# Kernel optimization log

Hardware: AMD Instinct MI355X
Metric: run time of the kernel (lower is better)

Reference implementation:

```python
import jax, jax.numpy as jnp
import numpy as np

N, E, D, K = 50000, 600000, 128, 8
EPS = 1e-09


def setup_inputs() -> dict:
    key = jax.random.key(0)
    ks = jax.random.split(key, 10)
    feature = jax.random.normal(ks[0], (N, D), dtype=jnp.float32)
    snorm_n = jax.random.uniform(ks[1], (N, 1), dtype=jnp.float32)
    src = jax.random.randint(ks[2], (E,), 0, N, dtype=jnp.int32)
    dst = jax.random.randint(ks[3], (E,), 0, N, dtype=jnp.int32)
    W_low = jax.random.normal(ks[4], (D, D), dtype=jnp.float32) / np.sqrt(D)
    W_high = jax.random.normal(ks[5], (D, D), dtype=jnp.float32) / np.sqrt(D)
    W_mid = jax.random.normal(ks[6], (D, D), dtype=jnp.float32) / np.sqrt(D)
    gamma_low = jax.random.uniform(ks[7], (K,), dtype=jnp.float32)
    gamma_high = jax.random.uniform(ks[8], (K,), dtype=jnp.float32)
    gamma_mid = jax.random.uniform(ks[9], (K,), dtype=jnp.float32)
    bias = jnp.zeros((D,), dtype=jnp.float32)
    return {"feature": feature, "snorm_n": snorm_n, "src": src, "dst": dst,
            "W_low": W_low, "W_high": W_high, "W_mid": W_mid,
            "gamma_low": gamma_low, "gamma_high": gamma_high,
            "gamma_mid": gamma_mid, "bias": bias}


def _mp(feat, src, dst, norm):
    # symmetric-normalized SpMM: h[v] = norm[v] * sum_{u->v} norm[u]*feat[u]
    msg = (feat * norm[:, None])[src]                        # [E, D] gather
    agg = jax.ops.segment_sum(msg, dst, num_segments=N)       # [N, D] scatter-add
    return agg * norm[:, None]


def reference(feature, snorm_n, src, dst, W_low, W_high, W_mid,
              gamma_low, gamma_high, gamma_mid, bias):
    deg = jax.ops.segment_sum(jnp.ones((E,), feature.dtype), dst, num_segments=N)
    norm = jnp.clip(deg, 1.0) ** -0.5                          # in-degree^-0.5
    alpha = jnp.linspace(EPS, 1.0 - EPS, K).astype(feature.dtype)
    midalpha = jnp.linspace(EPS, 1.0, K).astype(feature.dtype)

    h = _mp(feature, src, dst, norm)

    gl = jax.nn.relu(gamma_low)
    o0 = (jnp.dot(alpha, gl) * h + jnp.dot(1.0 - alpha, gl) * feature) @ W_low.T
    gh = jax.nn.relu(gamma_high)
    o1 = (jnp.dot(-alpha, gh) * h + jnp.dot(1.0 - alpha, gh) * feature) @ W_high.T
    gm = jax.nn.relu(gamma_mid)
    h1 = _mp(h, src, dst, norm)
    o2 = (jnp.sum(gm) * h1 - jnp.dot(midalpha, gm) * feature) @ W_mid.T

    # sequential mutual gating, exactly as the torch in-place updates
    o0 = o0 * jax.nn.sigmoid(o1 + o2)
    o1 = o1 * jax.nn.sigmoid(o0 + o2)
    o2 = o2 * jax.nn.sigmoid(o0 + o1)

    out = o0 + o1 + o2 + bias
    out = out * snorm_n          # graph_norm
    out = jax.nn.relu(out)       # activation
    return out
```

## Files before the change

### kernel.cpp

```cpp
#include <hip/hip_runtime.h>
#include <hip/hip_bf16.h>
#include <math.h>

#define N_NODES 50000
#define N_EDGES 600000
#define DIM 128
#define KGAM 8
#define EPSV 1e-9f
#define RBLK 3128
#define NTILES 1564
#define GGRID 512

typedef __attribute__((ext_vector_type(8))) short short8;
typedef __attribute__((ext_vector_type(4))) float float4v;

__device__ __forceinline__ short f2bf(float f) {
    return (short)__builtin_bit_cast(unsigned short, __float2bfloat16(f));
}
__device__ __forceinline__ unsigned int pack2(float a, float b) {
    return (unsigned int)(unsigned short)f2bf(a) | ((unsigned int)(unsigned short)f2bf(b) << 16);
}
__device__ __forceinline__ float sigm(float x) { return 1.f / (1.f + __expf(-x)); }

__global__ void k_deg(const int* __restrict__ dst, int* __restrict__ deg) {
    int e = blockIdx.x * blockDim.x + threadIdx.x;
    if (e < N_EDGES) atomicAdd(&deg[dst[e]], 1);
}

__global__ void k_scan1(const int* __restrict__ deg, int* __restrict__ rowstart,
                        int* __restrict__ bsums, float* __restrict__ norm) {
    __shared__ int s[256];
    int tid = threadIdx.x;
    int i0 = blockIdx.x * 1024 + tid * 4;
    int v[4]; int sum = 0;
#pragma unroll
    for (int c = 0; c < 4; ++c) {
        int i = i0 + c;
        int d = (i < N_NODES) ? deg[i] : 0;
        v[c] = d; sum += d;
    }
    s[tid] = sum; __syncthreads();
#pragma unroll
    for (int off = 1; off < 256; off <<= 1) {
        int t = (tid >= off) ? s[tid - off] : 0;
        __syncthreads();
        s[tid] += t;
        __syncthreads();
    }
    if (tid == 255) bsums[blockIdx.x] = s[255];
    int run = s[tid] - sum;
#pragma unroll
    for (int c = 0; c < 4; ++c) {
        int i = i0 + c;
        if (i < N_NODES) {
            rowstart[i] = run;
            norm[i] = rsqrtf((float)(v[c] < 1 ? 1 : v[c]));
        }
        run += v[c];
    }
}

__global__ void k_scan2(int* __restrict__ bsums, int nb) {
    __shared__ int s[64];
    int tid = threadIdx.x;
    int v = (tid < nb) ? bsums[tid] : 0;
    s[tid] = v; __syncthreads();
#pragma unroll
    for (int off = 1; off < 64; off <<= 1) {
        int t = (tid >= off) ? s[tid - off] : 0;
        __syncthreads();
        s[tid] += t;
        __syncthreads();
    }
    if (tid < nb) bsums[tid] = s[tid] - v;
}

__global__ void k_scan3(const int* __restrict__ bsums, int* __restrict__ rowstart) {
    int i = blockIdx.x * blockDim.x + threadIdx.x;
    if (i < N_NODES) rowstart[i] += bsums[i >> 10];
    if (i == 0) rowstart[N_NODES] = N_EDGES;
}

__global__ void k_fill(const int* __restrict__ src, const int* __restrict__ dst,
                       const int* __restrict__ rowstart, int* __restrict__ cnt,
                       int* __restrict__ esrc) {
    int e = blockIdx.x * blockDim.x + threadIdx.x;
    if (e < N_EDGES) {
        int d = dst[e];
        int slot = rowstart[d] + atomicAdd(&cnt[d], 1);
        esrc[slot] = src[e];
    }
}

__global__ void k_wconv(const float* __restrict__ W0, const float* __restrict__ W1,
                        const float* __restrict__ W2, const float* __restrict__ gl,
                        const float* __restrict__ gh, const float* __restrict__ gm,
                        unsigned int* __restrict__ Wb) {
    int g = blockIdx.y;
    float a0 = 0, b0 = 0, a1 = 0, b1 = 0, sg = 0, m2 = 0;
#pragma unroll
    for (int k = 0; k < KGAM; ++k) {
        float al = EPSV + (float)k * (1.f - 2.f * EPSV) / (KGAM - 1);
        float md = EPSV + (float)k * (1.f - EPSV) / (KGAM - 1);
        float l = fmaxf(gl[k], 0.f), h = fmaxf(gh[k], 0.f), m = fmaxf(gm[k], 0.f);
        a0 += al * l;  b0 += (1.f - al) * l;
        a1 += -al * h; b1 += (1.f - al) * h;
        sg += m;       m2 += md * m;
    }
    float cc[6] = {a0, b0, a1, b1, sg, -m2};
    float c = cc[g];
    const float* Ws = (g < 2) ? W0 : (g < 4) ? W1 : W2;
    int i = (blockIdx.x * 256 + threadIdx.x) * 4;
    if (i < DIM * DIM) {
        float4 v = *(const float4*)(Ws + i);
        uint2 o; o.x = pack2(c * v.x, c * v.y); o.y = pack2(c * v.z, c * v.w);
        *(uint2*)(Wb + (g * DIM * DIM + i) / 2) = o;
    }
}

__device__ __forceinline__ size_t tiled_off(int row, int k) {
    return (size_t)(row >> 4) * 2048 + ((k >> 5) << 9) + (((k >> 3) & 3) << 7)
         + ((row & 15) << 3) + (k & 7);
}

__global__ void k_prescale(const float4* __restrict__ f, const float* __restrict__ norm,
                           unsigned int* __restrict__ fb, uint2* __restrict__ fp) {
    int i = blockIdx.x * 256 + threadIdx.x;
    if (i >= N_NODES * DIM / 4) return;
    int row = i >> 5;
    int k0 = (i & 31) * 4;
    float nv = norm[row];
    float4 v = f[i];
    uint2 a; a.x = pack2(v.x, v.y); a.y = pack2(v.z, v.w);
    uint2 b; b.x = pack2(v.x * nv, v.y * nv); b.y = pack2(v.z * nv, v.w * nv);
    *(uint2*)(fb + tiled_off(row, k0) / 2) = a;
    fp[i] = b;
}

__device__ __forceinline__ void acc8(float* a, uint4 r) {
    a[0] += __builtin_bit_cast(float, r.x << 16);
    a[1] += __builtin_bit_cast(float, r.x & 0xffff0000u);
    a[2] += __builtin_bit_cast(float, r.y << 16);
    a[3] += __builtin_bit_cast(float, r.y & 0xffff0000u);
    a[4] += __builtin_bit_cast(float, r.z << 16);
    a[5] += __builtin_bit_cast(float, r.z & 0xffff0000u);
    a[6] += __builtin_bit_cast(float, r.w << 16);
    a[7] += __builtin_bit_cast(float, r.w & 0xffff0000u);
}

__global__ void k_spmm(const uint4* __restrict__ in, const float* __restrict__ norm,
                       const int* __restrict__ rowstart, const int* __restrict__ esrc,
                       uint4* __restrict__ hout, uint4* __restrict__ preout, int wpre) {
    int v = blockIdx.x * 16 + (threadIdx.x >> 4);
    int l = threadIdx.x & 15;
    if (v >= N_NODES) return;
    int beg = rowstart[v], end = rowstart[v + 1];
    float a[8] = {0.f, 0.f, 0.f, 0.f, 0.f, 0.f, 0.f, 0.f};
    int t = beg;
    for (; t + 7 < end; t += 8) {
        int u0 = esrc[t],     u1 = esrc[t + 1], u2 = esrc[t + 2], u3 = esrc[t + 3];
        int u4 = esrc[t + 4], u5 = esrc[t + 5], u6 = esrc[t + 6], u7 = esrc[t + 7];
        uint4 r0 = in[(size_t)u0 * 16 + l];
        uint4 r1 = in[(size_t)u1 * 16 + l];
        uint4 r2 = in[(size_t)u2 * 16 + l];
        uint4 r3 = in[(size_t)u3 * 16 + l];
        uint4 r4 = in[(size_t)u4 * 16 + l];
        uint4 r5 = in[(size_t)u5 * 16 + l];
        uint4 r6 = in[(size_t)u6 * 16 + l];
        uint4 r7 = in[(size_t)u7 * 16 + l];
        acc8(a, r0); acc8(a, r1); acc8(a, r2); acc8(a, r3);
        acc8(a, r4); acc8(a, r5); acc8(a, r6); acc8(a, r7);
    }
    if (t + 3 < end) {
        int u0 = esrc[t], u1 = esrc[t + 1], u2 = esrc[t + 2], u3 = esrc[t + 3];
        uint4 r0 = in[(size_t)u0 * 16 + l];
        uint4 r1 = in[(size_t)u1 * 16 + l];
        uint4 r2 = in[(size_t)u2 * 16 + l];
        uint4 r3 = in[(size_t)u3 * 16 + l];
        acc8(a, r0); acc8(a, r1); acc8(a, r2); acc8(a, r3);
        t += 4;
    }
    if (t + 1 < end) {
        int u0 = esrc[t], u1 = esrc[t + 1];
        uint4 r0 = in[(size_t)u0 * 16 + l];
        uint4 r1 = in[(size_t)u1 * 16 + l];
        acc8(a, r0); acc8(a, r1);
        t += 2;
    }
    if (t < end) {
        uint4 r = in[(size_t)esrc[t] * 16 + l];
        acc8(a, r);
    }
    float nv = norm[v];
    uint4 o;
    o.x = pack2(a[0] * nv, a[1] * nv); o.y = pack2(a[2] * nv, a[3] * nv);
    o.z = pack2(a[4] * nv, a[5] * nv); o.w = pack2(a[6] * nv, a[7] * nv);
    size_t tix = (size_t)(v >> 4) * 256 + (size_t)(l >> 2) * 64
               + (size_t)(l & 3) * 16 + (v & 15);
    hout[tix] = o;
    if (wpre) {
        float n2 = nv * nv;
        uint4 p;
        p.x = pack2(a[0] * n2, a[1] * n2); p.y = pack2(a[2] * n2, a[3] * n2);
        p.z = pack2(a[4] * n2, a[5] * n2); p.w = pack2(a[6] * n2, a[7] * n2);
        preout[(size_t)v * 16 + l] = p;
    }
}

typedef const __attribute__((address_space(1))) unsigned int* gp1_t;
typedef __attribute__((address_space(3))) unsigned int* lp3_t;

__global__ __launch_bounds__(512, 2) void k_gemm_fused(
    const short* __restrict__ hB, const short* __restrict__ fB,
    const short* __restrict__ h1B, const short* __restrict__ Wb,
    const float* __restrict__ bias, const float* __restrict__ snorm,
    float* __restrict__ out) {
    __shared__ short Ts[2][24 * 512];

    const int tid = threadIdx.x;
    const int lane = tid & 63;
    const int wv = tid >> 6;
    const int m = lane & 15;
    const int quad = lane >> 4;

    const int col = wv * 16 + m;
    const float bc = bias[col];
    const short* wp = Wb + (size_t)col * DIM + quad * 8;

    int t0 = blockIdx.x;
    {
#pragma unroll
        for (int i = 0; i < 3; ++i) {
            int s = wv * 3 + i;
            int g = s >> 3, rb = (s >> 2) & 1, ks = s & 3;
            const short* base = (g == 0) ? hB : (g == 1) ? fB : h1B;
            const short* gp = base + (size_t)(t0 * 2 + rb) * 2048 + ks * 512 + lane * 8;
            __builtin_amdgcn_global_load_lds((gp1_t)(const void*)gp,
                                             (lp3_t)(void*)&Ts[0][s * 512], 16, 0, 0);
        }
    }

    int buf = 0;
    for (int t = t0; t < NTILES; t += GGRID) {
        __syncthreads();

        int tn = t + GGRID;
        if (tn < NTILES) {
#pragma unroll
            for (int i = 0; i < 3; ++i) {
                int s = wv * 3 + i;
                int g = s >> 3, rb = (s >> 2) & 1, ks = s & 3;
                const short* base = (g == 0) ? hB : (g == 1) ? fB : h1B;
                const short* gp = base + (size_t)(tn * 2 + rb) * 2048 + ks * 512 + lane * 8;
                __builtin_amdgcn_global_load_lds((gp1_t)(const void*)gp,
                                                 (lp3_t)(void*)&Ts[buf ^ 1][s * 512], 16, 0, 0);
            }
        }

        float4v acc[3][2];
        const float4v zero = {0.f, 0.f, 0.f, 0.f};
#pragma unroll
        for (int g = 0; g < 3; ++g) {
            acc[g][0] = zero; acc[g][1] = zero;
        }

#pragma unroll
        for (int ks = 0; ks < 4; ++ks) {
            const short* wk = wp + ks * 32;
            short8 b0 = *(const short8*)(wk);
            short8 b1 = *(const short8*)(wk + DIM * DIM);
            short8 b2 = *(const short8*)(wk + 2 * DIM * DIM);
            short8 b3 = *(const short8*)(wk + 3 * DIM * DIM);
            short8 b4 = *(const short8*)(wk + 4 * DIM * DIM);
            short8 b5 = *(const short8*)(wk + 5 * DIM * DIM);
#pragma unroll
            for (int rb = 0; rb < 2; ++rb) {
                const short* ap = &Ts[buf][(rb * 4 + ks) * 512 + lane * 8];
                short8 x_h = *(const short8*)(ap);
                short8 x_f = *(const short8*)(ap + 8 * 512);
                short8 x_1 = *(const short8*)(ap + 16 * 512);
                acc[0][rb] = __builtin_amdgcn_mfma_f32_16x16x32_bf16(x_h, b0, acc[0][rb], 0, 0, 0);
                acc[0][rb] = __builtin_amdgcn_mfma_f32_16x16x32_bf16(x_f, b1, acc[0][rb], 0, 0, 0);
                acc[1][rb] = __builtin_amdgcn_mfma_f32_16x16x32_bf16(x_h, b2, acc[1][rb], 0, 0, 0);
                acc[1][rb] = __builtin_amdgcn_mfma_f32_16x16x32_bf16(x_f, b3, acc[1][rb], 0, 0, 0);
                acc[2][rb] = __builtin_amdgcn_mfma_f32_16x16x32_bf16(x_1, b4, acc[2][rb], 0, 0, 0);
                acc[2][rb] = __builtin_amdgcn_mfma_f32_16x16x32_bf16(x_f, b5, acc[2][rb], 0, 0, 0);
            }
        }

#pragma unroll
        for (int rb = 0; rb < 2; ++rb) {
#pragma unroll
            for (int r = 0; r < 4; ++r) {
                int row = t * 32 + rb * 16 + quad * 4 + r;
                if (row < N_NODES) {
                    float sn = snorm[row];
                    float o0 = acc[0][rb][r], o1 = acc[1][rb][r], o2 = acc[2][rb][r];
                    float g0 = o0 * sigm(o1 + o2);
                    float g1 = o1 * sigm(g0 + o2);
                    float g2 = o2 * sigm(g0 + g1);
                    float vv = (g0 + g1 + g2 + bc) * sn;
                    out[(size_t)row * DIM + col] = fmaxf(vv, 0.f);
                }
            }
        }
        buf ^= 1;
    }
}

extern "C" void kernel_launch(void* const* d_in, const int* in_sizes, int n_in,
                              void* d_out, int out_size, void* d_ws, size_t ws_size,
                              hipStream_t stream) {
    const float* feature = (const float*)d_in[0];
    const float* snorm   = (const float*)d_in[1];
    const int*   src     = (const int*)d_in[2];
    const int*   dst     = (const int*)d_in[3];
    const float* W_low   = (const float*)d_in[4];
    const float* W_high  = (const float*)d_in[5];
    const float* W_mid   = (const float*)d_in[6];
    const float* gl      = (const float*)d_in[7];
    const float* gh      = (const float*)d_in[8];
    const float* gm      = (const float*)d_in[9];
    const float* bias    = (const float*)d_in[10];
    float* out = (float*)d_out;

    char* w = (char*)d_ws;
    auto alloc = [&](size_t bytes) {
        char* p = w;
        w += (bytes + 255) & ~(size_t)255;
        return p;
    };
    const size_t tiledBytes = (size_t)RBLK * 2048 * 2;
    float* norm   = (float*)alloc((size_t)N_NODES * 4);
    int* deg      = (int*)alloc((size_t)2 * N_NODES * 4);
    int* cnt      = deg + N_NODES;
    int* rowstart = (int*)alloc((size_t)(N_NODES + 1) * 4);
    int* bsums    = (int*)alloc(64 * 4);
    int* esrc     = (int*)alloc((size_t)N_EDGES * 4);
    short* Wb     = (short*)alloc((size_t)6 * DIM * DIM * 2);
    short* fb     = (short*)alloc(tiledBytes);
    short* fp     = (short*)alloc((size_t)N_NODES * DIM * 2);
    short* h      = (short*)alloc(tiledBytes);
    short* hp     = (short*)alloc((size_t)N_NODES * DIM * 2);
    short* h1     = (short*)alloc(tiledBytes);

    hipMemsetAsync(deg, 0, (size_t)2 * N_NODES * 4, stream);
    k_deg<<<(N_EDGES + 255) / 256, 256, 0, stream>>>(dst, deg);
    int nchunks = (N_NODES + 1023) / 1024;
    k_scan1<<<nchunks, 256, 0, stream>>>(deg, rowstart, bsums, norm);
    k_scan2<<<1, 64, 0, stream>>>(bsums, nchunks);
    k_scan3<<<(N_NODES + 255) / 256, 256, 0, stream>>>(bsums, rowstart);
    k_fill<<<(N_EDGES + 255) / 256, 256, 0, stream>>>(src, dst, rowstart, cnt, esrc);
    k_wconv<<<dim3(16, 6), 256, 0, stream>>>(W_low, W_high, W_mid, gl, gh, gm,
                                             (unsigned int*)Wb);
    k_prescale<<<(N_NODES * DIM / 4 + 255) / 256, 256, 0, stream>>>(
        (const float4*)feature, norm, (unsigned int*)fb, (uint2*)fp);

    int spmm_blocks = (N_NODES + 15) / 16;
    k_spmm<<<spmm_blocks, 256, 0, stream>>>((const uint4*)fp, norm, rowstart, esrc,
                                            (uint4*)h, (uint4*)hp, 1);
    k_spmm<<<spmm_blocks, 256, 0, stream>>>((const uint4*)hp, norm, rowstart, esrc,
                                            (uint4*)h1, (uint4*)hp, 0);

    k_gemm_fused<<<GGRID, 512, 0, stream>>>(h, fb, h1, Wb, bias, snorm, out);
}
```

Before: 252.9 us.

## Split SpMM edges across wavefront subgroups and use one-tile-per-block GEMM

The SpMM now gives each node a full 64-lane wavefront. Four 16-lane groups each take an interleaved subset of the node's edges, and their partial sums are combined with cross-lane shuffles. This is meant to spread uneven in-degrees and expose more memory-level parallelism per node, at the cost of shuffle reductions and idle lanes on low-degree nodes. The fused GEMM drops the persistent double-buffered loop for a non-persistent grid of 256-thread blocks, one 32-row tile each, with each wave computing two column blocks. This trades prefetch overlap for higher occupancy and simpler scheduling.

```diff
diff --git a/kernel.cpp b/kernel.cpp
--- a/kernel.cpp
+++ b/kernel.cpp
@@ -9,7 +9,6 @@
 #define EPSV 1e-9f
 #define RBLK 3128
 #define NTILES 1564
-#define GGRID 512
 
 typedef __attribute__((ext_vector_type(8))) short short8;
 typedef __attribute__((ext_vector_type(4))) float float4v;
@@ -151,122 +150,97 @@
 __global__ void k_spmm(const uint4* __restrict__ in, const float* __restrict__ norm,
                        const int* __restrict__ rowstart, const int* __restrict__ esrc,
                        uint4* __restrict__ hout, uint4* __restrict__ preout, int wpre) {
-    int v = blockIdx.x * 16 + (threadIdx.x >> 4);
-    int l = threadIdx.x & 15;
+    int v = blockIdx.x * 4 + (threadIdx.x >> 6);
     if (v >= N_NODES) return;
+    int lane = threadIdx.x & 63;
+    int eg = lane >> 4;
+    int l = lane & 15;
     int beg = rowstart[v], end = rowstart[v + 1];
     float a[8] = {0.f, 0.f, 0.f, 0.f, 0.f, 0.f, 0.f, 0.f};
-    int t = beg;
-    for (; t + 7 < end; t += 8) {
-        int u0 = esrc[t],     u1 = esrc[t + 1], u2 = esrc[t + 2], u3 = esrc[t + 3];
-        int u4 = esrc[t + 4], u5 = esrc[t + 5], u6 = esrc[t + 6], u7 = esrc[t + 7];
-        uint4 r0 = in[(size_t)u0 * 16 + l];
-        uint4 r1 = in[(size_t)u1 * 16 + l];
-        uint4 r2 = in[(size_t)u2 * 16 + l];
-        uint4 r3 = in[(size_t)u3 * 16 + l];
-        uint4 r4 = in[(size_t)u4 * 16 + l];
-        uint4 r5 = in[(size_t)u5 * 16 + l];
-        uint4 r6 = in[(size_t)u6 * 16 + l];
-        uint4 r7 = in[(size_t)u7 * 16 + l];
-        acc8(a, r0); acc8(a, r1); acc8(a, r2); acc8(a, r3);
-        acc8(a, r4); acc8(a, r5); acc8(a, r6); acc8(a, r7);
-    }
-    if (t + 3 < end) {
-        int u0 = esrc[t], u1 = esrc[t + 1], u2 = esrc[t + 2], u3 = esrc[t + 3];
-        uint4 r0 = in[(size_t)u0 * 16 + l];
-        uint4 r1 = in[(size_t)u1 * 16 + l];
-        uint4 r2 = in[(size_t)u2 * 16 + l];
-        uint4 r3 = in[(size_t)u3 * 16 + l];
-        acc8(a, r0); acc8(a, r1); acc8(a, r2); acc8(a, r3);
-        t += 4;
-    }
-    if (t + 1 < end) {
-        int u0 = esrc[t], u1 = esrc[t + 1];
+    int e = beg + eg;
+    for (; e + 4 < end; e += 8) {
+        int u0 = esrc[e], u1 = esrc[e + 4];
         uint4 r0 = in[(size_t)u0 * 16 + l];
         uint4 r1 = in[(size_t)u1 * 16 + l];
         acc8(a, r0); acc8(a, r1);
-        t += 2;
-    }
-    if (t < end) {
-        uint4 r = in[(size_t)esrc[t] * 16 + l];
+    }
+    if (e < end) {
+        uint4 r = in[(size_t)esrc[e] * 16 + l];
         acc8(a, r);
     }
-    float nv = norm[v];
-    uint4 o;
-    o.x = pack2(a[0] * nv, a[1] * nv); o.y = pack2(a[2] * nv, a[3] * nv);
-    o.z = pack2(a[4] * nv, a[5] * nv); o.w = pack2(a[6] * nv, a[7] * nv);
-    size_t tix = (size_t)(v >> 4) * 256 + (size_t)(l >> 2) * 64
-               + (size_t)(l & 3) * 16 + (v & 15);
-    hout[tix] = o;
-    if (wpre) {
-        float n2 = nv * nv;
-        uint4 p;
-        p.x = pack2(a[0] * n2, a[1] * n2); p.y = pack2(a[2] * n2, a[3] * n2);
-        p.z = pack2(a[4] * n2, a[5] * n2); p.w = pack2(a[6] * n2, a[7] * n2);
-        preout[(size_t)v * 16 + l] = p;
+#pragma unroll
+    for (int j = 0; j < 8; ++j) {
+        a[j] += __shfl_xor(a[j], 16, 64);
+        a[j] += __shfl_xor(a[j], 32, 64);
+    }
+    if (eg == 0) {
+        float nv = norm[v];
+        uint4 o;
+        o.x = pack2(a[0] * nv, a[1] * nv); o.y = pack2(a[2] * nv, a[3] * nv);
+        o.z = pack2(a[4] * nv, a[5] * nv); o.w = pack2(a[6] * nv, a[7] * nv);
+        size_t tix = (size_t)(v >> 4) * 256 + (size_t)(l >> 2) * 64
+                   + (size_t)(l & 3) * 16 + (v & 15);
+        hout[tix] = o;
+        if (wpre) {
+            float n2 = nv * nv;
+            uint4 p;
+            p.x = pack2(a[0] * n2, a[1] * n2); p.y = pack2(a[2] * n2, a[3] * n2);
+            p.z = pack2(a[4] * n2, a[5] * n2); p.w = pack2(a[6] * n2, a[7] * n2);
+            preout[(size_t)v * 16 + l] = p;
+        }
     }
 }
 
 typedef const __attribute__((address_space(1))) unsigned int* gp1_t;
 typedef __attribute__((address_space(3))) unsigned int* lp3_t;
 
-__global__ __launch_bounds__(512, 2) void k_gemm_fused(
+__global__ __launch_bounds__(256, 4) void k_gemm_fused(
     const short* __restrict__ hB, const short* __restrict__ fB,
     const short* __restrict__ h1B, const short* __restrict__ Wb,
     const float* __restrict__ bias, const float* __restrict__ snorm,
     float* __restrict__ out) {
-    __shared__ short Ts[2][24 * 512];
+    __shared__ short Ts[24 * 512];
 
     const int tid = threadIdx.x;
     const int lane = tid & 63;
     const int wv = tid >> 6;
     const int m = lane & 15;
     const int quad = lane >> 4;
-
-    const int col = wv * 16 + m;
-    const float bc = bias[col];
-    const short* wp = Wb + (size_t)col * DIM + quad * 8;
-
-    int t0 = blockIdx.x;
-    {
-#pragma unroll
-        for (int i = 0; i < 3; ++i) {
-            int s = wv * 3 + i;
-            int g = s >> 3, rb = (s >> 2) & 1, ks = s & 3;
-            const short* base = (g == 0) ? hB : (g == 1) ? fB : h1B;
-            const short* gp = base + (size_t)(t0 * 2 + rb) * 2048 + ks * 512 + lane * 8;
-            __builtin_amdgcn_global_load_lds((gp1_t)(const void*)gp,
-                                             (lp3_t)(void*)&Ts[0][s * 512], 16, 0, 0);
-        }
-    }
-
-    int buf = 0;
-    for (int t = t0; t < NTILES; t += GGRID) {
-        __syncthreads();
-
-        int tn = t + GGRID;
-        if (tn < NTILES) {
-#pragma unroll
-            for (int i = 0; i < 3; ++i) {
-                int s = wv * 3 + i;
-                int g = s >> 3, rb = (s >> 2) & 1, ks = s & 3;
-                const short* base = (g == 0) ? hB : (g == 1) ? fB : h1B;
-                const short* gp = base + (size_t)(tn * 2 + rb) * 2048 + ks * 512 + lane * 8;
-                __builtin_amdgcn_global_load_lds((gp1_t)(const void*)gp,
-                                                 (lp3_t)(void*)&Ts[buf ^ 1][s * 512], 16, 0, 0);
-            }
-        }
-
-        float4v acc[3][2];
-        const float4v zero = {0.f, 0.f, 0.f, 0.f};
-#pragma unroll
-        for (int g = 0; g < 3; ++g) {
-            acc[g][0] = zero; acc[g][1] = zero;
-        }
-
-#pragma unroll
-        for (int ks = 0; ks < 4; ++ks) {
-            const short* wk = wp + ks * 32;
+    const int r0 = blockIdx.x * 32;
+
+#pragma unroll
+    for (int i = 0; i < 6; ++i) {
+        int s = wv * 6 + i;
+        int g = s >> 3, rb = (s >> 2) & 1, ks = s & 3;
+        const short* base = (g == 0) ? hB : (g == 1) ? fB : h1B;
+        const short* gp = base + (size_t)(blockIdx.x * 2 + rb) * 2048 + ks * 512 + lane * 8;
+        __builtin_amdgcn_global_load_lds((gp1_t)(const void*)gp,
+                                         (lp3_t)(void*)&Ts[s * 512], 16, 0, 0);
+    }
+    __syncthreads();
+
+    float4v acc[3][2][2];
+    const float4v zero = {0.f, 0.f, 0.f, 0.f};
+#pragma unroll
+    for (int g = 0; g < 3; ++g)
+#pragma unroll
+        for (int rb = 0; rb < 2; ++rb) {
+            acc[g][rb][0] = zero; acc[g][rb][1] = zero;
+        }
+
+#pragma unroll
+    for (int ks = 0; ks < 4; ++ks) {
+        short8 xh[2], xf[2], x1[2];
+#pragma unroll
+        for (int rb = 0; rb < 2; ++rb) {
+            const short* ap = &Ts[(rb * 4 + ks) * 512 + lane * 8];
+            xh[rb] = *(const short8*)(ap);
+            xf[rb] = *(const short8*)(ap + 8 * 512);
+            x1[rb] = *(const short8*)(ap + 16 * 512);
+        }
+#pragma unroll
+        for (int c = 0; c < 2; ++c) {
+            const short* wk = Wb + (size_t)((wv * 2 + c) * 16 + m) * DIM + quad * 8 + ks * 32;
             short8 b0 = *(const short8*)(wk);
             short8 b1 = *(const short8*)(wk + DIM * DIM);
             short8 b2 = *(const short8*)(wk + 2 * DIM * DIM);
@@ -275,36 +249,35 @@
             short8 b5 = *(const short8*)(wk + 5 * DIM * DIM);
 #pragma unroll
             for (int rb = 0; rb < 2; ++rb) {
-                const short* ap = &Ts[buf][(rb * 4 + ks) * 512 + lane * 8];
-                short8 x_h = *(const short8*)(ap);
-                short8 x_f = *(const short8*)(ap + 8 * 512);
-                short8 x_1 = *(const short8*)(ap + 16 * 512);
-                acc[0][rb] = __builtin_amdgcn_mfma_f32_16x16x32_bf16(x_h, b0, acc[0][rb], 0, 0, 0);
-                acc[0][rb] = __builtin_amdgcn_mfma_f32_16x16x32_bf16(x_f, b1, acc[0][rb], 0, 0, 0);
-                acc[1][rb] = __builtin_amdgcn_mfma_f32_16x16x32_bf16(x_h, b2, acc[1][rb], 0, 0, 0);
-                acc[1][rb] = __builtin_amdgcn_mfma_f32_16x16x32_bf16(x_f, b3, acc[1][rb], 0, 0, 0);
-                acc[2][rb] = __builtin_amdgcn_mfma_f32_16x16x32_bf16(x_1, b4, acc[2][rb], 0, 0, 0);
-                acc[2][rb] = __builtin_amdgcn_mfma_f32_16x16x32_bf16(x_f, b5, acc[2][rb], 0, 0, 0);
+                acc[0][rb][c] = __builtin_amdgcn_mfma_f32_16x16x32_bf16(xh[rb], b0, acc[0][rb][c], 0, 0, 0);
+                acc[0][rb][c] = __builtin_amdgcn_mfma_f32_16x16x32_bf16(xf[rb], b1, acc[0][rb][c], 0, 0, 0);
+                acc[1][rb][c] = __builtin_amdgcn_mfma_f32_16x16x32_bf16(xh[rb], b2, acc[1][rb][c], 0, 0, 0);
+                acc[1][rb][c] = __builtin_amdgcn_mfma_f32_16x16x32_bf16(xf[rb], b3, acc[1][rb][c], 0, 0, 0);
+                acc[2][rb][c] = __builtin_amdgcn_mfma_f32_16x16x32_bf16(x1[rb], b4, acc[2][rb][c], 0, 0, 0);
+                acc[2][rb][c] = __builtin_amdgcn_mfma_f32_16x16x32_bf16(xf[rb], b5, acc[2][rb][c], 0, 0, 0);
             }
         }
-
-#pragma unroll
-        for (int rb = 0; rb < 2; ++rb) {
-#pragma unroll
-            for (int r = 0; r < 4; ++r) {
-                int row = t * 32 + rb * 16 + quad * 4 + r;
-                if (row < N_NODES) {
-                    float sn = snorm[row];
-                    float o0 = acc[0][rb][r], o1 = acc[1][rb][r], o2 = acc[2][rb][r];
+    }
+
+#pragma unroll
+    for (int rb = 0; rb < 2; ++rb) {
+#pragma unroll
+        for (int r = 0; r < 4; ++r) {
+            int row = r0 + rb * 16 + quad * 4 + r;
+            if (row < N_NODES) {
+                float sn = snorm[row];
+#pragma unroll
+                for (int c = 0; c < 2; ++c) {
+                    int col = (wv * 2 + c) * 16 + m;
+                    float o0 = acc[0][rb][c][r], o1 = acc[1][rb][c][r], o2 = acc[2][rb][c][r];
                     float g0 = o0 * sigm(o1 + o2);
                     float g1 = o1 * sigm(g0 + o2);
                     float g2 = o2 * sigm(g0 + g1);
-                    float vv = (g0 + g1 + g2 + bc) * sn;
+                    float vv = (g0 + g1 + g2 + bias[col]) * sn;
                     out[(size_t)row * DIM + col] = fmaxf(vv, 0.f);
                 }
             }
         }
-        buf ^= 1;
     }
 }
 
@@ -356,11 +329,11 @@
     k_prescale<<<(N_NODES * DIM / 4 + 255) / 256, 256, 0, stream>>>(
         (const float4*)feature, norm, (unsigned int*)fb, (uint2*)fp);
 
-    int spmm_blocks = (N_NODES + 15) / 16;
+    int spmm_blocks = (N_NODES + 3) / 4;
     k_spmm<<<spmm_blocks, 256, 0, stream>>>((const uint4*)fp, norm, rowstart, esrc,
                                             (uint4*)h, (uint4*)hp, 1);
     k_spmm<<<spmm_blocks, 256, 0, stream>>>((const uint4*)hp, norm, rowstart, esrc,
                                             (uint4*)h1, (uint4*)hp, 0);
 
-    k_gemm_fused<<<GGRID, 512, 0, stream>>>(h, fb, h1, Wb, bias, snorm, out);
-}
+    k_gemm_fused<<<NTILES, 256, 0, stream>>>(h, fb, h1, Wb, bias, snorm, out);
+}
```

Measured after the change: 274.0 us. +8.3%, slower.
